# Kernel tuning notes

Hardware: AMD Instinct MI355X
Metric: run time of the kernel (lower is better)

Reference implementation:

```python
import math
import jax, jax.numpy as jnp
import numpy as np

N_HEADS = 8
WINDOW = 4


def _get_relative_embeddings(emb, length, window):
    # emb: [1, 2*window+1, k_channels] -> [1, 2*length-1, k_channels]
    pad_length = max(length - (window + 1), 0)
    start = max(window + 1 - length, 0)
    if pad_length > 0:
        emb = jnp.pad(emb, ((0, 0), (pad_length, pad_length), (0, 0)))
    return emb[:, start:start + 2 * length - 1]


def _relative_position_to_absolute_position(x):
    # x: [b, h, l, 2l-1] -> [b, h, l, l] (skewing trick)
    b, h, l, _ = x.shape
    x = jnp.pad(x, ((0, 0), (0, 0), (0, 0), (0, 1)))
    x_flat = x.reshape(b, h, l * 2 * l)
    x_flat = jnp.pad(x_flat, ((0, 0), (0, 0), (0, l - 1)))
    return x_flat.reshape(b, h, l + 1, 2 * l - 1)[:, :, :l, l - 1:]


def _absolute_position_to_relative_position(x):
    # x: [b, h, l, l] -> [b, h, l, 2l-1]
    b, h, l, _ = x.shape
    x = jnp.pad(x, ((0, 0), (0, 0), (0, 0), (0, l - 1)))
    x_flat = x.reshape(b, h, l * l + l * (l - 1))
    x_flat = jnp.pad(x_flat, ((0, 0), (0, 0), (l, 0)))
    return x_flat.reshape(b, h, l, 2 * l)[:, :, :, 1:]


def setup_inputs() -> dict:
    key = jax.random.key(0)
    ks = jax.random.split(key, 12)
    b, t, d = 4, 1024, 512
    kc = d // N_HEADS
    s = 1.0 / math.sqrt(d)
    return {
        "x": jax.random.normal(ks[0], (b, t, d), jnp.float32),
        "c": jax.random.normal(ks[1], (b, t, d), jnp.float32),
        "wq": jax.random.normal(ks[2], (d, d), jnp.float32) * s,
        "bq": jnp.zeros((d,), jnp.float32),
        "wk": jax.random.normal(ks[3], (d, d), jnp.float32) * s,
        "bk": jnp.zeros((d,), jnp.float32),
        "wv": jax.random.normal(ks[4], (d, d), jnp.float32) * s,
        "bv": jnp.zeros((d,), jnp.float32),
        "wo": jax.random.normal(ks[5], (d, d), jnp.float32) * s,
        "bo": jnp.zeros((d,), jnp.float32),
        "emb_rel_k": jax.random.normal(ks[6], (1, 2 * WINDOW + 1, kc), jnp.float32) * kc ** -0.5,
        "emb_rel_v": jax.random.normal(ks[7], (1, 2 * WINDOW + 1, kc), jnp.float32) * kc ** -0.5,
    }


def reference(x, c, wq, bq, wk, bk, wv, bv, wo, bo, emb_rel_k, emb_rel_v):
    b, t, d = x.shape
    h = N_HEADS
    kc = d // h
    inv_sqrt = 1.0 / math.sqrt(kc)

    # 1x1 conv projections (pointwise matmul)
    q = x @ wq + bq   # [b, t, d]
    k = c @ wk + bk
    v = c @ wv + bv

    # Faithful reshape as in source: [b, t, d] -> [b, h, kc, t] -> [b, h, t, kc]
    q = q.reshape(b, h, kc, t).transpose(0, 1, 3, 2)
    k = k.reshape(b, h, kc, t).transpose(0, 1, 3, 2)
    v = v.reshape(b, h, kc, t).transpose(0, 1, 3, 2)

    scores = jnp.einsum('bhtd,bhsd->bhts', q, k) * inv_sqrt  # [b,h,t,t]

    # relative key logits
    key_rel = _get_relative_embeddings(emb_rel_k, t, WINDOW)[0]  # [2t-1, kc]
    rel_logits = jnp.einsum('bhtd,md->bhtm', q, key_rel)          # [b,h,t,2t-1]
    scores_local = _relative_position_to_absolute_position(rel_logits) * inv_sqrt
    scores = scores + scores_local

    p_attn = jax.nn.softmax(scores, axis=-1)
    output = jnp.einsum('bhts,bhsd->bhtd', p_attn, v)  # [b,h,t,kc]

    # relative value contribution
    rel_weights = _absolute_position_to_relative_position(p_attn)  # [b,h,t,2t-1]
    val_rel = _get_relative_embeddings(emb_rel_v, t, WINDOW)[0]    # [2t-1, kc]
    output = output + jnp.einsum('bhtm,md->bhtd', rel_weights, val_rel)

    # Faithful output reshape: [b,h,t,kc] -> [b,h,kc,t] -> [b,t,d]
    output = output.transpose(0, 1, 3, 2).reshape(b, t, d)
    out = output @ wo + bo
    return out
```

## Files before the change

### kernel.cpp

```cpp
#include <hip/hip_runtime.h>
#include <hip/hip_bf16.h>

#define NB 4
#define NT 1024
#define ND 512
#define NH 8
#define NKC 64

typedef __bf16 bf16x8 __attribute__((ext_vector_type(8)));
typedef float f32x4 __attribute__((ext_vector_type(4)));

__device__ __forceinline__ f32x4 MFMA(bf16x8 a, bf16x8 b, f32x4 c) {
    return __builtin_amdgcn_mfma_f32_16x16x32_bf16(a, b, c, 0, 0, 0);
}
__device__ __forceinline__ unsigned short f2bu(float v) {
    __hip_bfloat16 b = __float2bfloat16(v);
    return *(unsigned short*)&b;
}
__device__ __forceinline__ void split1(float v, unsigned short& h, unsigned short& l)
{
    __hip_bfloat16 hb = __float2bfloat16(v);
    float r = v - __bfloat162float(hb);
    __hip_bfloat16 lb = __float2bfloat16(r);
    h = *(unsigned short*)&hb;
    l = *(unsigned short*)&lb;
}
__device__ __forceinline__ void splitpack(const float4 a, const float4 b, uint4& h, uint4& l)
{
    union { unsigned short u[8]; uint4 v; } H, L;
    const float f[8] = {a.x, a.y, a.z, a.w, b.x, b.y, b.z, b.w};
    #pragma unroll
    for (int j = 0; j < 8; ++j) split1(f[j], H.u[j], L.u[j]);
    h = H.v; l = L.v;
}

__global__ __launch_bounds__(256)
void splitT_kernel(const float* __restrict__ w0, const float* __restrict__ w1,
                   const float* __restrict__ w2, const float* __restrict__ w3,
                   unsigned short* __restrict__ wT)
{
    __shared__ float tl[32][33];
    const float* w = (blockIdx.z == 0) ? w0 : (blockIdx.z == 1) ? w1
                   : (blockIdx.z == 2) ? w2 : w3;
    unsigned short* hi = wT + (size_t)blockIdx.z * 2 * (ND * ND);
    unsigned short* lo = hi + ND * ND;
    const int t = threadIdx.x;
    const int x0 = blockIdx.x * 32, y0 = blockIdx.y * 32;
    {
        const int r = t >> 3, c = (t & 7) * 4;
        const float4 v = *(const float4*)&w[(size_t)(y0 + r) * ND + x0 + c];
        tl[r][c] = v.x; tl[r][c+1] = v.y; tl[r][c+2] = v.z; tl[r][c+3] = v.w;
    }
    __syncthreads();
    {
        const int nr = t >> 3, k4 = (t & 7) * 4;
        unsigned short hh[4], ll[4];
        #pragma unroll
        for (int j = 0; j < 4; ++j) split1(tl[k4 + j][nr], hh[j], ll[j]);
        ushort4 h = make_ushort4(hh[0], hh[1], hh[2], hh[3]);
        ushort4 l = make_ushort4(ll[0], ll[1], ll[2], ll[3]);
        *(ushort4*)&hi[(size_t)(x0 + nr) * ND + y0 + k4] = h;
        *(ushort4*)&lo[(size_t)(x0 + nr) * ND + y0 + k4] = l;
    }
}

__global__ __launch_bounds__(256, 3)
void proj_mfma(const float* __restrict__ x, const float* __restrict__ cc,
               const unsigned short* __restrict__ wT,
               const float* __restrict__ bq, const float* __restrict__ bk,
               const float* __restrict__ bv,
               unsigned short* __restrict__ qh_o, unsigned short* __restrict__ ql_o,
               unsigned short* __restrict__ kh_o, unsigned short* __restrict__ vh_o)
{
    __shared__ unsigned short smem[12288];
    unsigned short* Ah = smem;
    unsigned short* Al = smem + 2048;
    unsigned short* Bh = smem + 4096;
    unsigned short* Bl = smem + 8192;
    unsigned short* Tr = smem;

    const int which = blockIdx.z;
    const float* A_g = (which == 0) ? x : cc;
    const unsigned short* Bh_g = wT + (size_t)which * 2 * (ND * ND);
    const unsigned short* Bl_g = Bh_g + ND * ND;
    const float* bias = (which == 0) ? bq : (which == 1) ? bk : bv;

    const int tid = threadIdx.x, l = tid & 63, w = tid >> 6;
    const int quad = l >> 4, lc = l & 15;
    const int wm = w & 1, wn = w >> 1;
    const int n0 = blockIdx.x * 128, m0 = blockIdx.y * 64;

    const int am = tid >> 2, ak = (tid & 3) * 8;
    const size_t aG = (size_t)(m0 + am) * ND + ak;
    const int bn = tid >> 1, bk2 = (tid & 1) * 16;
    const size_t bG = (size_t)(n0 + bn) * ND + bk2;

    float4 ra0 = *(const float4*)&A_g[aG];
    float4 ra1 = *(const float4*)&A_g[aG + 4];
    uint4 rb0 = *(const uint4*)&Bh_g[bG];
    uint4 rb1 = *(const uint4*)&Bh_g[bG + 8];
    uint4 rb2 = {}, rb3 = {};
    if (which != 2) {
        rb2 = *(const uint4*)&Bl_g[bG];
        rb3 = *(const uint4*)&Bl_g[bG + 8];
    }

    f32x4 acc[2][4];
    #pragma unroll
    for (int mi = 0; mi < 2; ++mi)
        #pragma unroll
        for (int ni = 0; ni < 4; ++ni) acc[mi][ni] = (f32x4){0.f, 0.f, 0.f, 0.f};

    for (int k0 = 0; k0 < ND; k0 += 32) {
        __syncthreads();
        {
            uint4 h0, l0;
            splitpack(ra0, ra1, h0, l0);
            *(uint4*)&Ah[am * 32 + ak] = h0;
            *(uint4*)&Al[am * 32 + ak] = l0;
            *(uint4*)&Bh[bn * 32 + bk2] = rb0; *(uint4*)&Bh[bn * 32 + bk2 + 8] = rb1;
            if (which != 2) {
                *(uint4*)&Bl[bn * 32 + bk2] = rb2; *(uint4*)&Bl[bn * 32 + bk2 + 8] = rb3;
            }
        }
        __syncthreads();
        if (k0 + 32 < ND) {
            const size_t aN = aG + k0 + 32, bN = bG + k0 + 32;
            ra0 = *(const float4*)&A_g[aN];
            ra1 = *(const float4*)&A_g[aN + 4];
            rb0 = *(const uint4*)&Bh_g[bN];
            rb1 = *(const uint4*)&Bh_g[bN + 8];
            if (which != 2) {
                rb2 = *(const uint4*)&Bl_g[bN];
                rb3 = *(const uint4*)&Bl_g[bN + 8];
            }
        }

        bf16x8 ah[2], al2[2], bh[4], bl[4];
        #pragma unroll
        for (int mi = 0; mi < 2; ++mi) {
            const int ar = (wm * 32 + mi * 16 + lc) * 32 + quad * 8;
            ah[mi] = *(const bf16x8*)&Ah[ar];
            al2[mi] = *(const bf16x8*)&Al[ar];
        }
        #pragma unroll
        for (int ni = 0; ni < 4; ++ni) {
            const int br = (wn * 64 + ni * 16 + lc) * 32 + quad * 8;
            bh[ni] = *(const bf16x8*)&Bh[br];
            if (which != 2) bl[ni] = *(const bf16x8*)&Bl[br];
        }
        if (which != 2) {
            #pragma unroll
            for (int mi = 0; mi < 2; ++mi)
                #pragma unroll
                for (int ni = 0; ni < 4; ++ni) {
                    acc[mi][ni] = MFMA(al2[mi], bh[ni], acc[mi][ni]);
                    acc[mi][ni] = MFMA(ah[mi], bl[ni], acc[mi][ni]);
                    acc[mi][ni] = MFMA(ah[mi], bh[ni], acc[mi][ni]);
                }
        } else {
            #pragma unroll
            for (int mi = 0; mi < 2; ++mi)
                #pragma unroll
                for (int ni = 0; ni < 4; ++ni) {
                    acc[mi][ni] = MFMA(al2[mi], bh[ni], acc[mi][ni]);
                    acc[mi][ni] = MFMA(ah[mi], bh[ni], acc[mi][ni]);
                }
        }
    }

    const int bb = m0 >> 10, tt0 = m0 & 1023;
    const int hh = tt0 >> 7, cch0 = (tt0 & 127) >> 1;
    const int bh_idx = bb * NH + hh;

    if (which == 2) {
        #pragma unroll
        for (int ni = 0; ni < 4; ++ni) {
            const int n = n0 + wn * 64 + ni * 16 + lc;
            const float bval = bias[n];
            #pragma unroll
            for (int mi = 0; mi < 2; ++mi)
                #pragma unroll
                for (int r = 0; r < 4; ++r) {
                    const int mloc = wm * 32 + mi * 16 + quad * 4 + r;
                    const int cch = cch0 + (mloc >> 1);
                    const int t = (mloc & 1) * 512 + n;
                    vh_o[(((size_t)bh_idx * 16 + (t >> 6)) * 64 + cch) * 64 + (t & 63)] =
                        f2bu(acc[mi][ni][r] + bval);
                }
        }
        return;
    }

    const int npass = (which == 0) ? 2 : 1;
    unsigned short* outp[2] = {(which == 0) ? qh_o : kh_o, ql_o};

    for (int pass = 0; pass < npass; ++pass) {
        __syncthreads();
        #pragma unroll
        for (int ni = 0; ni < 4; ++ni) {
            const int nloc = wn * 64 + ni * 16 + lc;
            const float bval = bias[n0 + nloc];
            #pragma unroll
            for (int mi = 0; mi < 2; ++mi)
                #pragma unroll
                for (int r = 0; r < 4; ++r) {
                    const int mloc = wm * 32 + mi * 16 + quad * 4 + r;
                    const float val = acc[mi][ni][r] + bval;
                    unsigned short hs, ls;
                    if (which == 0) { split1(val, hs, ls); }
                    else { hs = f2bu(val); ls = 0; }
                    Tr[((mloc & 1) * 128 + nloc) * 40 + (mloc >> 1)] =
                        (pass == 0) ? hs : ls;
                }
        }
        __syncthreads();
        {
            const int t = (tid >> 7) * 512 + n0 + (tid & 127);
            const size_t oa = ((size_t)bh_idx * NT + t) * NKC + cch0;
            const uint4 v0 = *(const uint4*)&Tr[tid * 40];
            const uint4 v1 = *(const uint4*)&Tr[tid * 40 + 8];
            const uint4 v2 = *(const uint4*)&Tr[tid * 40 + 16];
            const uint4 v3 = *(const uint4*)&Tr[tid * 40 + 24];
            *(uint4*)&outp[pass][oa]      = v0;
            *(uint4*)&outp[pass][oa + 8]  = v1;
            *(uint4*)&outp[pass][oa + 16] = v2;
            *(uint4*)&outp[pass][oa + 24] = v3;
        }
    }
}

__global__ __launch_bounds__(256, 4)
void attn_mfma(const unsigned short* __restrict__ qh_g, const unsigned short* __restrict__ ql_g,
               const unsigned short* __restrict__ kh_g,
               const unsigned short* __restrict__ vh_g,
               const float* __restrict__ embk, const float* __restrict__ embv,
               float* __restrict__ O0, float* __restrict__ O1,
               float* __restrict__ l0_g, float* __restrict__ l1_g)
{
    __shared__ unsigned short smem[19456];
    unsigned short* KsH = smem;
    unsigned short* Vt  = smem + 4608;
    unsigned short* Ps  = smem + 11264;
    float* bandv = (float*)(smem + 17920);
    unsigned short* EkH = smem + 11264;

    const int tid = threadIdx.x, l = tid & 63, w = tid >> 6;
    const int quad = l >> 4, lc = l & 15;
    const int q0 = (blockIdx.x >> 1) * 64;
    const int sh = blockIdx.x & 1;
    const int sBeg = sh * 512;
    const int hh = blockIdx.y, bb = blockIdx.z;
    const int bh = bb * NH + hh;
    const size_t qkBase = (size_t)bh * NT * NKC;
    const size_t vtBase = (size_t)bh * (16 * 64 * 64);
    float* Op = sh ? O1 : O0;
    float* lp = sh ? l1_g : l0_g;

    const int srow = tid >> 2, sseg = (tid & 3) * 16;

    auto loadKV = [&](uint4& k0r, uint4& k1r, uint4& v0r, uint4& v1r, int tile) {
        const size_t ka = qkBase + (size_t)(sBeg + tile * 64 + srow) * NKC + sseg;
        const size_t va = vtBase + (size_t)((sBeg >> 6) + tile) * 4096 + srow * 64 + sseg;
        k0r = *(const uint4*)&kh_g[ka];
        k1r = *(const uint4*)&kh_g[ka + 8];
        v0r = *(const uint4*)&vh_g[va];
        v1r = *(const uint4*)&vh_g[va + 8];
    };

    uint4 ak0, ak1, av0, av1, bk0, bk1, bv0, bv1;
    loadKV(ak0, ak1, av0, av1, 0);
    loadKV(bk0, bk1, bv0, bv1, 1);

    for (int idx = tid; idx < 16 * 72; idx += 256) {
        const int d = idx / 72, kc = idx - d * 72;
        EkH[idx] = f2bu((d < 9 && kc < 64) ? embk[d * 64 + kc] : 0.f);
    }
    for (int idx = tid; idx < 64 * 40; idx += 256) {
        const int c = idx / 40, col = 64 + (idx - c * 40);
        const int d = col - 64;
        Vt[c * 104 + col] = f2bu((d < 9) ? embv[d * 64 + c] : 0.f);
    }
    __syncthreads();

    bf16x8 qh[2], ql[2];
    {
        const int qg = q0 + w * 16 + lc;
        const size_t qa = qkBase + (size_t)qg * NKC + quad * 8;
        qh[0] = *(const bf16x8*)&qh_g[qa];
        qh[1] = *(const bf16x8*)&qh_g[qa + 32];
        ql[0] = *(const bf16x8*)&ql_g[qa];
        ql[1] = *(const bf16x8*)&ql_g[qa + 32];
    }

    {
        f32x4 accB = (f32x4){0.f, 0.f, 0.f, 0.f};
        #pragma unroll
        for (int kk = 0; kk < 2; ++kk) {
            const bf16x8 ebh = *(const bf16x8*)&EkH[lc * 72 + kk * 32 + quad * 8];
            accB = MFMA(ql[kk], ebh, accB);
            accB = MFMA(qh[kk], ebh, accB);
        }
        __syncthreads();
        if (lc <= 8) {
            #pragma unroll
            for (int r = 0; r < 4; ++r)
                bandv[(w * 16 + quad * 4 + r) * 12 + lc] = accB[r];
        }
    }
    unsigned short* P = Ps + w * 1664;
    {
        const int zr = l >> 2, zc = 80 + (l & 3) * 4;
        *(ushort4*)&P[zr * 104 + zc] = make_ushort4(0, 0, 0, 0);
    }

    f32x4 O[4];
    #pragma unroll
    for (int ci = 0; ci < 4; ++ci) O[ci] = (f32x4){0.f, 0.f, 0.f, 0.f};
    float l_run[4] = {0.f, 0.f, 0.f, 0.f};

    auto tilestep = [&](uint4& k0r, uint4& k1r, uint4& v0r, uint4& v1r,
                        int i, int nextTile) {
        const int s0 = sBeg + i * 64;
        __syncthreads();
        *(uint4*)&KsH[srow * 72 + sseg]      = k0r;
        *(uint4*)&KsH[srow * 72 + sseg + 8]  = k1r;
        *(uint4*)&Vt[srow * 104 + sseg]      = v0r;
        *(uint4*)&Vt[srow * 104 + sseg + 8]  = v1r;
        __syncthreads();
        if (nextTile >= 0) loadKV(k0r, k1r, v0r, v1r, nextTile);

        f32x4 S[4];
        #pragma unroll
        for (int ni = 0; ni < 4; ++ni) {
            f32x4 a = (f32x4){0.f, 0.f, 0.f, 0.f};
            #pragma unroll
            for (int kk = 0; kk < 2; ++kk) {
                const bf16x8 kb = *(const bf16x8*)&KsH[(ni * 16 + lc) * 72 + kk * 32 + quad * 8];
                a = MFMA(ql[kk], kb, a);
                a = MFMA(qh[kk], kb, a);
            }
            S[ni] = a;
        }

        #pragma unroll
        for (int ni = 0; ni < 4; ++ni)
            #pragma unroll
            for (int r = 0; r < 4; ++r) {
                const int ql64 = w * 16 + quad * 4 + r;
                const int dp4 = (s0 + ni * 16 + lc) - (q0 + ql64) + 4;
                float sv = S[ni][r];
                if (dp4 >= 0 && dp4 <= 8) sv += bandv[ql64 * 12 + dp4];
                S[ni][r] = __expf(sv * 0.125f);
            }
        #pragma unroll
        for (int r = 0; r < 4; ++r)
            l_run[r] += S[0][r] + S[1][r] + S[2][r] + S[3][r];

        {
            const int zr = l >> 2, zc = 64 + (l & 3) * 4;
            *(ushort4*)&P[zr * 104 + zc] = make_ushort4(0, 0, 0, 0);
        }
        #pragma unroll
        for (int ni = 0; ni < 4; ++ni)
            #pragma unroll
            for (int r = 0; r < 4; ++r) {
                const int prow = quad * 4 + r;
                const unsigned short pb = f2bu(S[ni][r]);
                P[prow * 104 + ni * 16 + lc] = pb;
                const int dp4 = (s0 + ni * 16 + lc) - (q0 + w * 16 + prow) + 4;
                if (dp4 >= 0 && dp4 <= 8) P[prow * 104 + 64 + dp4] = pb;
            }

        #pragma unroll
        for (int ks = 0; ks < 3; ++ks) {
            const bf16x8 pa = *(const bf16x8*)&P[lc * 104 + ks * 32 + quad * 8];
            #pragma unroll
            for (int ci = 0; ci < 4; ++ci) {
                const bf16x8 vb = *(const bf16x8*)&Vt[(ci * 16 + lc) * 104 + ks * 32 + quad * 8];
                O[ci] = MFMA(pa, vb, O[ci]);
            }
        }
    };

    for (int ii = 0; ii < 8; ii += 2) {
        tilestep(ak0, ak1, av0, av1, ii,     (ii + 2 < 8) ? ii + 2 : -1);
        tilestep(bk0, bk1, bv0, bv1, ii + 1, (ii + 3 < 8) ? ii + 3 : -1);
    }

    #pragma unroll
    for (int r = 0; r < 4; ++r) {
        float v = l_run[r];
        v += __shfl_xor(v, 1); v += __shfl_xor(v, 2);
        v += __shfl_xor(v, 4); v += __shfl_xor(v, 8);
        l_run[r] = v;
    }
    const int qg0 = q0 + w * 16 + quad * 4;
    if (lc == 0) {
        #pragma unroll
        for (int r = 0; r < 4; ++r)
            lp[(size_t)bh * NT + qg0 + r] = l_run[r];
    }
    #pragma unroll
    for (int ci = 0; ci < 4; ++ci) {
        const int c = ci * 16 + lc;
        *(f32x4*)&Op[((size_t)bh * 64 + c) * NT + qg0] = O[ci];
    }
}

__global__ __launch_bounds__(256, 4)
void outproj_fused(const float* __restrict__ O0, const float* __restrict__ O1,
                   const float* __restrict__ l0_g, const float* __restrict__ l1_g,
                   const unsigned short* __restrict__ wTh,
                   const float* __restrict__ bo, float* __restrict__ out)
{
    __shared__ unsigned short As[64 * 32], Bh[64 * 32], Bl[64 * 32];
    __shared__ float linv[1024];
    const unsigned short* Bl_g = wTh + ND * ND;
    const int tid = threadIdx.x, l = tid & 63, w = tid >> 6;
    const int quad = l >> 4, lc = l & 15;
    const int wm = w & 1, wn = w >> 1;
    const int n0 = blockIdx.x * 64, m0 = blockIdx.y * 64;

    const int bb = m0 >> 10, hh = (m0 & 1023) >> 7;
    const int bh = bb * NH + hh;

    for (int i = tid; i < 1024; i += 256)
        linv[i] = 1.f / (l0_g[(size_t)bh * NT + i] + l1_g[(size_t)bh * NT + i]);

    const int sm = tid >> 2, sk = (tid & 3) * 8;
    const int cch = ((m0 & 127) + sm) >> 1, tb = sm & 1;
    const size_t oBase = ((size_t)bh * 64 + cch) * NT + tb * 512 + sk;
    const size_t bG = (size_t)(n0 + sm) * ND + sk;

    float4 ro0a = *(const float4*)&O0[oBase];
    float4 ro0b = *(const float4*)&O0[oBase + 4];
    float4 ro1a = *(const float4*)&O1[oBase];
    float4 ro1b = *(const float4*)&O1[oBase + 4];
    uint4 rbh = *(const uint4*)&wTh[bG];
    uint4 rbl = *(const uint4*)&Bl_g[bG];

    f32x4 acc[2][2];
    #pragma unroll
    for (int mi = 0; mi < 2; ++mi)
        #pragma unroll
        for (int ni = 0; ni < 2; ++ni) acc[mi][ni] = (f32x4){0.f, 0.f, 0.f, 0.f};

    for (int k0 = 0; k0 < ND; k0 += 32) {
        __syncthreads();
        {
            const float* lv = &linv[tb * 512 + k0 + sk];
            const float f[8] = {ro0a.x + ro1a.x, ro0a.y + ro1a.y,
                                ro0a.z + ro1a.z, ro0a.w + ro1a.w,
                                ro0b.x + ro1b.x, ro0b.y + ro1b.y,
                                ro0b.z + ro1b.z, ro0b.w + ro1b.w};
            union { unsigned short u[8]; uint4 v; } pk;
            #pragma unroll
            for (int j = 0; j < 8; ++j) pk.u[j] = f2bu(f[j] * lv[j]);
            *(uint4*)&As[sm * 32 + sk] = pk.v;
            *(uint4*)&Bh[sm * 32 + sk] = rbh;
            *(uint4*)&Bl[sm * 32 + sk] = rbl;
        }
        __syncthreads();
        if (k0 + 32 < ND) {
            ro0a = *(const float4*)&O0[oBase + k0 + 32];
            ro0b = *(const float4*)&O0[oBase + k0 + 36];
            ro1a = *(const float4*)&O1[oBase + k0 + 32];
            ro1b = *(const float4*)&O1[oBase + k0 + 36];
            rbh  = *(const uint4*)&wTh[bG + k0 + 32];
            rbl  = *(const uint4*)&Bl_g[bG + k0 + 32];
        }
        bf16x8 ab[2], bhf[2], blf[2];
        #pragma unroll
        for (int mi = 0; mi < 2; ++mi)
            ab[mi] = *(const bf16x8*)&As[(wm * 32 + mi * 16 + lc) * 32 + quad * 8];
        #pragma unroll
        for (int ni = 0; ni < 2; ++ni) {
            const int br = (wn * 32 + ni * 16 + lc) * 32 + quad * 8;
            bhf[ni] = *(const bf16x8*)&Bh[br];
            blf[ni] = *(const bf16x8*)&Bl[br];
        }
        #pragma unroll
        for (int mi = 0; mi < 2; ++mi)
            #pragma unroll
            for (int ni = 0; ni < 2; ++ni) {
                acc[mi][ni] = MFMA(ab[mi], bhf[ni], acc[mi][ni]);
                acc[mi][ni] = MFMA(ab[mi], blf[ni], acc[mi][ni]);
            }
    }

    #pragma unroll
    for (int ni = 0; ni < 2; ++ni) {
        const int n = n0 + wn * 32 + ni * 16 + lc;
        const float bval = bo[n];
        #pragma unroll
        for (int mi = 0; mi < 2; ++mi)
            #pragma unroll
            for (int r = 0; r < 4; ++r) {
                const int m = m0 + wm * 32 + mi * 16 + quad * 4 + r;
                out[(size_t)m * ND + n] = acc[mi][ni][r] + bval;
            }
    }
}

extern "C" void kernel_launch(void* const* d_in, const int* in_sizes, int n_in,
                              void* d_out, int out_size, void* d_ws, size_t ws_size,
                              hipStream_t stream) {
    const float* x    = (const float*)d_in[0];
    const float* c    = (const float*)d_in[1];
    const float* wq   = (const float*)d_in[2];
    const float* bq   = (const float*)d_in[3];
    const float* wk   = (const float*)d_in[4];
    const float* bk   = (const float*)d_in[5];
    const float* wv   = (const float*)d_in[6];
    const float* bv   = (const float*)d_in[7];
    const float* wo   = (const float*)d_in[8];
    const float* bo   = (const float*)d_in[9];
    const float* embk = (const float*)d_in[10];
    const float* embv = (const float*)d_in[11];

    unsigned short* u16 = (unsigned short*)d_ws;
    const size_t M = 1024 * 1024;
    unsigned short* wT  = u16;
    unsigned short* qh  = u16 + 2 * M;
    unsigned short* ql  = u16 + 4 * M;
    unsigned short* kh  = u16 + 6 * M;
    unsigned short* vh  = u16 + 8 * M;
    float* fbase = (float*)(u16 + 10 * M);
    float* O0   = fbase;
    float* O1   = fbase + 2 * M;
    float* l0_g = fbase + 4 * M;
    float* l1_g = l0_g + 32768;

    splitT_kernel<<<dim3(16, 16, 4), 256, 0, stream>>>(wq, wk, wv, wo, wT);

    proj_mfma<<<dim3(4, 64, 3), 256, 0, stream>>>(x, c, wT, bq, bk, bv,
                                                  qh, ql, kh, vh);

    attn_mfma<<<dim3(32, 8, 4), 256, 0, stream>>>(qh, ql, kh, vh,
                                                  embk, embv, O0, O1, l0_g, l1_g);

    outproj_fused<<<dim3(8, 64), 256, 0, stream>>>(O0, O1, l0_g, l1_g,
                                                   wT + (size_t)3 * 2 * ND * ND,
                                                   bo, (float*)d_out);
}
```

Before: 171.1 us.

## Split combine into its own kernel, coalesce attention output stores, prefetch splitpack

Attention output tiles are now staged through shared memory so each row of O is written with contiguous vector stores instead of scattered 16-byte writes. A new combine kernel sums the two partial outputs, normalizes by the softmax denominators and writes a bf16 activation matrix in output-projection layout. The output projection then becomes a plain bf16 GEMM that no longer recomputes the reciprocal for 1024 rows in every block or reads two fp32 buffers. The projection GEMM also converts the next A tile to hi/lo bf16 after the MFMAs instead of before the shared-memory store. The trade-off is an extra kernel launch and an extra round trip through global memory for the bf16 intermediate.

```diff
diff --git a/kernel.cpp b/kernel.cpp
--- a/kernel.cpp
+++ b/kernel.cpp
@@ -104,6 +104,8 @@
         rb2 = *(const uint4*)&Bl_g[bG];
         rb3 = *(const uint4*)&Bl_g[bG + 8];
     }
+    uint4 sh0, sl0;
+    splitpack(ra0, ra1, sh0, sl0);
 
     f32x4 acc[2][4];
     #pragma unroll
@@ -114,17 +116,16 @@
     for (int k0 = 0; k0 < ND; k0 += 32) {
         __syncthreads();
         {
-            uint4 h0, l0;
-            splitpack(ra0, ra1, h0, l0);
-            *(uint4*)&Ah[am * 32 + ak] = h0;
-            *(uint4*)&Al[am * 32 + ak] = l0;
+            *(uint4*)&Ah[am * 32 + ak] = sh0;
+            *(uint4*)&Al[am * 32 + ak] = sl0;
             *(uint4*)&Bh[bn * 32 + bk2] = rb0; *(uint4*)&Bh[bn * 32 + bk2 + 8] = rb1;
             if (which != 2) {
                 *(uint4*)&Bl[bn * 32 + bk2] = rb2; *(uint4*)&Bl[bn * 32 + bk2 + 8] = rb3;
             }
         }
         __syncthreads();
-        if (k0 + 32 < ND) {
+        const bool hasNext = (k0 + 32 < ND);
+        if (hasNext) {
             const size_t aN = aG + k0 + 32, bN = bG + k0 + 32;
             ra0 = *(const float4*)&A_g[aN];
             ra1 = *(const float4*)&A_g[aN + 4];
@@ -167,6 +168,7 @@
                     acc[mi][ni] = MFMA(ah[mi], bh[ni], acc[mi][ni]);
                 }
         }
+        if (hasNext) splitpack(ra0, ra1, sh0, sl0);
     }
 
     const int bb = m0 >> 10, tt0 = m0 & 1023;
@@ -401,42 +403,71 @@
         for (int r = 0; r < 4; ++r)
             lp[(size_t)bh * NT + qg0 + r] = l_run[r];
     }
-    #pragma unroll
-    for (int ci = 0; ci < 4; ++ci) {
-        const int c = ci * 16 + lc;
-        *(f32x4*)&Op[((size_t)bh * 64 + c) * NT + qg0] = O[ci];
-    }
+    float* Os = (float*)smem;
+    __syncthreads();
+    #pragma unroll
+    for (int ci = 0; ci < 4; ++ci)
+        #pragma unroll
+        for (int r = 0; r < 4; ++r)
+            Os[(ci * 16 + lc) * 68 + w * 16 + quad * 4 + r] = O[ci][r];
+    __syncthreads();
+    {
+        const int c = tid >> 2, q4 = (tid & 3) * 16;
+        const size_t ob = ((size_t)bh * 64 + c) * NT + q0 + q4;
+        #pragma unroll
+        for (int i4 = 0; i4 < 16; i4 += 4)
+            *(f32x4*)&Op[ob + i4] = *(const f32x4*)&Os[c * 68 + q4 + i4];
+    }
+}
+
+__global__ __launch_bounds__(256)
+void combine_kernel(const float* __restrict__ O0, const float* __restrict__ O1,
+                    const float* __restrict__ l0_g, const float* __restrict__ l1_g,
+                    unsigned short* __restrict__ ath)
+{
+    const int q0 = blockIdx.x * 64, hh = blockIdx.y, bb = blockIdx.z;
+    const int bh = bb * NH + hh;
+    const int tid = threadIdx.x;
+    __shared__ float linv[64];
+    if (tid < 64)
+        linv[tid] = 1.f / (l0_g[(size_t)bh * NT + q0 + tid] +
+                           l1_g[(size_t)bh * NT + q0 + tid]);
+    __syncthreads();
+
+    const int c = tid >> 2, qq = (tid & 3) * 16;
+    const size_t ib = ((size_t)bh * 64 + c) * NT + q0 + qq;
+    union { unsigned short u[16]; uint4 v[2]; } out;
+    #pragma unroll
+    for (int j = 0; j < 16; j += 4) {
+        const f32x4 a = *(const f32x4*)&O0[ib + j];
+        const f32x4 b = *(const f32x4*)&O1[ib + j];
+        #pragma unroll
+        for (int r = 0; r < 4; ++r)
+            out.u[j + r] = f2bu((a[r] + b[r]) * linv[qq + j + r]);
+    }
+    const int row = hh * 128 + 2 * c + (q0 >> 9);
+    const size_t oa = ((size_t)bb * NT + row) * ND + (q0 & 511) + qq;
+    *(uint4*)&ath[oa]     = out.v[0];
+    *(uint4*)&ath[oa + 8] = out.v[1];
 }
 
 __global__ __launch_bounds__(256, 4)
-void outproj_fused(const float* __restrict__ O0, const float* __restrict__ O1,
-                   const float* __restrict__ l0_g, const float* __restrict__ l1_g,
-                   const unsigned short* __restrict__ wTh,
-                   const float* __restrict__ bo, float* __restrict__ out)
+void outproj_mfma(const unsigned short* __restrict__ a_g,
+                  const unsigned short* __restrict__ wTh,
+                  const float* __restrict__ bo, float* __restrict__ out)
 {
     __shared__ unsigned short As[64 * 32], Bh[64 * 32], Bl[64 * 32];
-    __shared__ float linv[1024];
     const unsigned short* Bl_g = wTh + ND * ND;
     const int tid = threadIdx.x, l = tid & 63, w = tid >> 6;
     const int quad = l >> 4, lc = l & 15;
     const int wm = w & 1, wn = w >> 1;
     const int n0 = blockIdx.x * 64, m0 = blockIdx.y * 64;
 
-    const int bb = m0 >> 10, hh = (m0 & 1023) >> 7;
-    const int bh = bb * NH + hh;
-
-    for (int i = tid; i < 1024; i += 256)
-        linv[i] = 1.f / (l0_g[(size_t)bh * NT + i] + l1_g[(size_t)bh * NT + i]);
-
     const int sm = tid >> 2, sk = (tid & 3) * 8;
-    const int cch = ((m0 & 127) + sm) >> 1, tb = sm & 1;
-    const size_t oBase = ((size_t)bh * 64 + cch) * NT + tb * 512 + sk;
+    const size_t aG = (size_t)(m0 + sm) * ND + sk;
     const size_t bG = (size_t)(n0 + sm) * ND + sk;
 
-    float4 ro0a = *(const float4*)&O0[oBase];
-    float4 ro0b = *(const float4*)&O0[oBase + 4];
-    float4 ro1a = *(const float4*)&O1[oBase];
-    float4 ro1b = *(const float4*)&O1[oBase + 4];
+    uint4 ra  = *(const uint4*)&a_g[aG];
     uint4 rbh = *(const uint4*)&wTh[bG];
     uint4 rbl = *(const uint4*)&Bl_g[bG];
 
@@ -448,27 +479,14 @@
 
     for (int k0 = 0; k0 < ND; k0 += 32) {
         __syncthreads();
-        {
-            const float* lv = &linv[tb * 512 + k0 + sk];
-            const float f[8] = {ro0a.x + ro1a.x, ro0a.y + ro1a.y,
-                                ro0a.z + ro1a.z, ro0a.w + ro1a.w,
-                                ro0b.x + ro1b.x, ro0b.y + ro1b.y,
-                                ro0b.z + ro1b.z, ro0b.w + ro1b.w};
-            union { unsigned short u[8]; uint4 v; } pk;
-            #pragma unroll
-            for (int j = 0; j < 8; ++j) pk.u[j] = f2bu(f[j] * lv[j]);
-            *(uint4*)&As[sm * 32 + sk] = pk.v;
-            *(uint4*)&Bh[sm * 32 + sk] = rbh;
-            *(uint4*)&Bl[sm * 32 + sk] = rbl;
-        }
+        *(uint4*)&As[sm * 32 + sk] = ra;
+        *(uint4*)&Bh[sm * 32 + sk] = rbh;
+        *(uint4*)&Bl[sm * 32 + sk] = rbl;
         __syncthreads();
         if (k0 + 32 < ND) {
-            ro0a = *(const float4*)&O0[oBase + k0 + 32];
-            ro0b = *(const float4*)&O0[oBase + k0 + 36];
-            ro1a = *(const float4*)&O1[oBase + k0 + 32];
-            ro1b = *(const float4*)&O1[oBase + k0 + 36];
-            rbh  = *(const uint4*)&wTh[bG + k0 + 32];
-            rbl  = *(const uint4*)&Bl_g[bG + k0 + 32];
+            ra  = *(const uint4*)&a_g[aG + k0 + 32];
+            rbh = *(const uint4*)&wTh[bG + k0 + 32];
+            rbl = *(const uint4*)&Bl_g[bG + k0 + 32];
         }
         bf16x8 ab[2], bhf[2], blf[2];
         #pragma unroll
@@ -526,7 +544,8 @@
     unsigned short* ql  = u16 + 4 * M;
     unsigned short* kh  = u16 + 6 * M;
     unsigned short* vh  = u16 + 8 * M;
-    float* fbase = (float*)(u16 + 10 * M);
+    unsigned short* ath = u16 + 10 * M;
+    float* fbase = (float*)(u16 + 12 * M);
     float* O0   = fbase;
     float* O1   = fbase + 2 * M;
     float* l0_g = fbase + 4 * M;
@@ -540,7 +559,9 @@
     attn_mfma<<<dim3(32, 8, 4), 256, 0, stream>>>(qh, ql, kh, vh,
                                                   embk, embv, O0, O1, l0_g, l1_g);
 
-    outproj_fused<<<dim3(8, 64), 256, 0, stream>>>(O0, O1, l0_g, l1_g,
-                                                   wT + (size_t)3 * 2 * ND * ND,
-                                                   bo, (float*)d_out);
-}
+    combine_kernel<<<dim3(16, 8, 4), 256, 0, stream>>>(O0, O1, l0_g, l1_g, ath);
+
+    outproj_mfma<<<dim3(8, 64), 256, 0, stream>>>(ath,
+                                                  wT + (size_t)3 * 2 * ND * ND,
+                                                  bo, (float*)d_out);
+}
```

Result: no change. 171.2 us (+0.1%).
